# Performance work log

Hardware: AMD Instinct MI355X
Metric: run time of the kernel (lower is better)

Reference implementation:

```python
import jax, jax.numpy as jnp
import numpy as np

ALPHA = 0.2  # dt/tau leaky-integration constant from the module (self._alpha)


def setup_inputs() -> dict:
    key = jax.random.key(0)
    ks = jax.random.split(key, 4)
    B, T, I, H, O = 64, 2048, 128, 512, 64
    inputs = jax.random.normal(ks[0], (B, T, I), dtype=jnp.float32)
    # Xavier-ish scales for weights
    W_in = jax.random.normal(ks[1], (H, I), dtype=jnp.float32) / np.sqrt(I)
    b_in = jnp.zeros((H,), dtype=jnp.float32)
    W_rec = jax.random.normal(ks[2], (H, H), dtype=jnp.float32) * (1.2 / np.sqrt(H))
    h_bias = jnp.zeros((H,), dtype=jnp.float32)
    W_out = jax.random.normal(ks[3], (O, H), dtype=jnp.float32) * (0.1 / np.sqrt(H))
    b_out = jnp.zeros((O,), dtype=jnp.float32)
    return {"inputs": inputs, "W_in": W_in, "b_in": b_in, "W_rec": W_rec,
            "h_bias": h_bias, "W_out": W_out, "b_out": b_out}


def reference(inputs, W_in, b_in, W_rec, h_bias, W_out, b_out):
    # inputs: [B, T, I] -> outputs: [B, T, O]
    B, T, I = inputs.shape
    H = W_rec.shape[0]
    # Precompute input projection for all timesteps: [B, T, H]
    x_proj = jnp.einsum('bti,hi->bth', inputs, W_in) + b_in
    h0 = jnp.zeros((B, H), dtype=inputs.dtype)

    def step(h, xp_t):
        # xp_t: [B, H] precomputed input_proj(x_t)
        h_raw = jnp.tanh(xp_t + h @ W_rec.T + h_bias)
        h_new = (1.0 - ALPHA) * h + ALPHA * h_raw
        return h_new, h_new

    # scan over time-major input projections
    _, hs = jax.lax.scan(step, h0, jnp.swapaxes(x_proj, 0, 1))  # hs: [T, B, H]
    hs = jnp.swapaxes(hs, 0, 1)  # [B, T, H]
    outputs = jnp.einsum('bth,oh->bto', hs, W_out) + b_out
    return outputs
```

## Files before the change

kernel.cpp:

```cpp
#include <hip/hip_runtime.h>


#define TT 2048
#define II 128
#define HH 512
#define OO 64

typedef unsigned long long u64;

union PW { u64 u; float f[2]; unsigned w[2]; };

__device__ __forceinline__ float dot4(float acc, float4 a, float4 w) {
    acc = fmaf(a.x, w.x, acc);
    acc = fmaf(a.y, w.y, acc);
    acc = fmaf(a.z, w.z, acc);
    acc = fmaf(a.w, w.w, acc);
    return acc;
}

__device__ __forceinline__ float fast_tanh(float x) {
    float ax = fabsf(x);
    float e  = __expf(-2.0f * ax);
    float r  = (1.0f - e) * __builtin_amdgcn_rcpf(1.0f + e);
    return copysignf(r, x);
}

__launch_bounds__(512, 1)
__global__ void rnn_persistent(const float* __restrict__ inputs,
                               const float* __restrict__ W_in,
                               const float* __restrict__ b_in,
                               const float* __restrict__ W_rec,
                               const float* __restrict__ h_bias,
                               const float* __restrict__ W_out,
                               const float* __restrict__ b_out,
                               float* __restrict__ out,
                               u64* __restrict__ gbufs)
{
    const int tid = (int)threadIdx.x;
    const int bid = (int)blockIdx.x;

    const int xcd = bid & 7;
    const int idx = bid >> 3;
    const int c   = idx & 3;
    const int g   = xcd * 8 + (idx >> 2);

    u64* gb0 = gbufs + (size_t)g * 1024;

    const int ksl = tid & 7;
    const int jp  = tid >> 3;
    const int j0  = c * 128 + jp * 2;
    const int j1  = j0 + 1;
    const int o   = c * 16 + (tid >> 5);
    const int ol  = tid & 31;

    __shared__ __align__(16) float hx[2][8][68];
    __shared__ __align__(16) float xt[2][8][20];

    float4 wr0[16], wr1[16];
#pragma unroll
    for (int q = 0; q < 16; ++q) {
        wr0[q] = *(const float4*)(W_rec + (size_t)j0 * HH + ksl * 64 + q * 4);
        wr1[q] = *(const float4*)(W_rec + (size_t)j1 * HH + ksl * 64 + q * 4);
    }
    float4 wi0[4], wi1[4];
#pragma unroll
    for (int q = 0; q < 4; ++q) {
        wi0[q] = *(const float4*)(W_in + (size_t)j0 * II + ksl * 16 + q * 4);
        wi1[q] = *(const float4*)(W_in + (size_t)j1 * II + ksl * 16 + q * 4);
    }
    float4 wo[4];
#pragma unroll
    for (int q = 0; q < 4; ++q)
        wo[q] = *(const float4*)(W_out + (size_t)o * HH + ol * 16 + q * 4);

    const float bias0 = b_in[j0] + h_bias[j0];
    const float bias1 = b_in[j1] + h_bias[j1];
    const float bo    = b_out[o];

    hx[0][tid >> 6][tid & 63] = 0.f;

    float hp0 = 0.f, hp1 = 0.f;

    const float* xptr = inputs + (size_t)g * TT * II + (tid & 127);
    float xv = 0.f;
    if (tid < 128) {
        xt[0][tid >> 4][tid & 15] = xptr[0];
        xv = xptr[II];
    }

    const int gm = (((c + 1 + (tid >> 7)) & 3) << 7) | (tid & 127);

    long budget = 1L << 20;

    __syncthreads();

    for (int t = 0; t < TT; ++t) {
        const int p = t & 1;
        u64* gb = gb0 + p * 512;
        const unsigned tag = (unsigned)(t + 1);

        float a0 = 0.f, a1 = 0.f;
        {
            const float4* hc = (const float4*)&hx[p][ksl][0];
#pragma unroll
            for (int q = 0; q < 16; ++q) {
                const float4 hv = hc[q];
                a0 = dot4(a0, hv, wr0[q]);
                a1 = dot4(a1, hv, wr1[q]);
            }
        }
        {
            const float4* xc = (const float4*)&xt[p][ksl][0];
#pragma unroll
            for (int q = 0; q < 4; ++q) {
                const float4 x4 = xc[q];
                a0 = dot4(a0, x4, wi0[q]);
                a1 = dot4(a1, x4, wi1[q]);
            }
        }
#pragma unroll
        for (int m = 1; m < 8; m <<= 1) {
            a0 += __shfl_xor(a0, m);
            a1 += __shfl_xor(a1, m);
        }

        hp0 = 0.8f * hp0 + 0.2f * fast_tanh(a0 + bias0);
        hp1 = 0.8f * hp1 + 0.2f * fast_tanh(a1 + bias1);

        if (ksl == 0) {
            PW w; w.f[0] = hp0; w.w[1] = tag;
            __hip_atomic_store(gb + j0, w.u, __ATOMIC_RELAXED, __HIP_MEMORY_SCOPE_AGENT);
        } else if (ksl == 1) {
            PW w; w.f[0] = hp1; w.w[1] = tag;
            __hip_atomic_store(gb + j1, w.u, __ATOMIC_RELAXED, __HIP_MEMORY_SCOPE_AGENT);
        } else if (ksl == 2) {
            float* dst = &hx[p ^ 1][j0 >> 6][j0 & 63];
            dst[0] = hp0;
            dst[1] = hp1;
        }
        asm volatile("" ::: "memory");

        if (t > 0) {
            float po = 0.f;
            const float4* hq = (const float4*)&hx[p][ol >> 2][(ol & 3) * 16];
#pragma unroll
            for (int q = 0; q < 4; ++q) po = dot4(po, hq[q], wo[q]);
#pragma unroll
            for (int m = 1; m < 32; m <<= 1) po += __shfl_xor(po, m);
            if (ol == 0) out[((size_t)g * TT + (t - 1)) * OO + o] = po + bo;
        }

        if (tid < 128) {
            xt[p ^ 1][tid >> 4][tid & 15] = xv;
            const int tn = (t + 2 < TT) ? (t + 2) : (TT - 1);
            xv = xptr[(size_t)tn * II];
        }

        if (tid < 384) {
            const u64* src = gb + gm;
            PW w;
            w.u = __hip_atomic_load(src, __ATOMIC_RELAXED, __HIP_MEMORY_SCOPE_AGENT);
            while (w.w[1] != tag) {
                __builtin_amdgcn_s_sleep(1);
                w.u = __hip_atomic_load(src, __ATOMIC_RELAXED, __HIP_MEMORY_SCOPE_AGENT);
                if (--budget < 0) break;
            }
            hx[p ^ 1][gm >> 6][gm & 63] = w.f[0];
        }
        __syncthreads();
    }

    {
        float po = 0.f;
        const float4* hq = (const float4*)&hx[0][ol >> 2][(ol & 3) * 16];
#pragma unroll
        for (int q = 0; q < 4; ++q) po = dot4(po, hq[q], wo[q]);
#pragma unroll
        for (int m = 1; m < 32; m <<= 1) po += __shfl_xor(po, m);
        if (ol == 0) out[((size_t)g * TT + (TT - 1)) * OO + o] = po + bo;
    }
}

extern "C" void kernel_launch(void* const* d_in, const int* in_sizes, int n_in,
                              void* d_out, int out_size, void* d_ws, size_t ws_size,
                              hipStream_t stream) {
    const float* inputs = (const float*)d_in[0];
    const float* W_in   = (const float*)d_in[1];
    const float* b_in   = (const float*)d_in[2];
    const float* W_rec  = (const float*)d_in[3];
    const float* h_bias = (const float*)d_in[4];
    const float* W_out  = (const float*)d_in[5];
    const float* b_out  = (const float*)d_in[6];
    float* out = (float*)d_out;

    u64* gbufs = (u64*)d_ws;
    hipMemsetAsync(d_ws, 0, 64 * 2 * 512 * sizeof(u64), stream);
    rnn_persistent<<<256, 512, 0, stream>>>(inputs, W_in, b_in, W_rec, h_bias,
                                            W_out, b_out, out, gbufs);
}
```

Before: 3.464 ms.

## Switch RNN state, weights and exchange to fp16 with fdot2 accumulation

Converts the register-resident weights, the shared hidden-state and input tiles, and the cross-block exchanged hidden values to fp16, and does the dot products with fdot2 (fp32 accumulation). Each global exchange word now packs two hidden values plus the tag, which halves the number of polling threads and spin loads per step. The sleep in the spin-wait is also removed to cut handoff latency. Storing the recurrent state in fp16 over 2048 steps risks accumulated precision error.

```diff
diff --git a/kernel.cpp b/kernel.cpp
--- a/kernel.cpp
+++ b/kernel.cpp
@@ -7,15 +7,28 @@
 #define OO 64
 
 typedef unsigned long long u64;
-
-union PW { u64 u; float f[2]; unsigned w[2]; };
-
-__device__ __forceinline__ float dot4(float acc, float4 a, float4 w) {
-    acc = fmaf(a.x, w.x, acc);
-    acc = fmaf(a.y, w.y, acc);
-    acc = fmaf(a.z, w.z, acc);
-    acc = fmaf(a.w, w.w, acc);
+typedef _Float16 h2_t __attribute__((ext_vector_type(2)));
+typedef _Float16 h8_t __attribute__((ext_vector_type(8)));
+
+union PW { u64 u; unsigned w[2]; _Float16 h[4]; };
+
+__device__ __forceinline__ float dot8(float acc, h8_t a, h8_t b) {
+    h2_t a0 = {a[0], a[1]}, a1 = {a[2], a[3]}, a2 = {a[4], a[5]}, a3 = {a[6], a[7]};
+    h2_t b0 = {b[0], b[1]}, b1 = {b[2], b[3]}, b2 = {b[4], b[5]}, b3 = {b[6], b[7]};
+    acc = __builtin_amdgcn_fdot2(a0, b0, acc, false);
+    acc = __builtin_amdgcn_fdot2(a1, b1, acc, false);
+    acc = __builtin_amdgcn_fdot2(a2, b2, acc, false);
+    acc = __builtin_amdgcn_fdot2(a3, b3, acc, false);
     return acc;
+}
+
+__device__ __forceinline__ h8_t cvt8(const float* p) {
+    const float4 lo = *(const float4*)p;
+    const float4 hi = *(const float4*)(p + 4);
+    h8_t r;
+    r[0] = (_Float16)lo.x; r[1] = (_Float16)lo.y; r[2] = (_Float16)lo.z; r[3] = (_Float16)lo.w;
+    r[4] = (_Float16)hi.x; r[5] = (_Float16)hi.y; r[6] = (_Float16)hi.z; r[7] = (_Float16)hi.w;
+    return r;
 }
 
 __device__ __forceinline__ float fast_tanh(float x) {
@@ -44,7 +57,7 @@
     const int c   = idx & 3;
     const int g   = xcd * 8 + (idx >> 2);
 
-    u64* gb0 = gbufs + (size_t)g * 1024;
+    u64* gb0 = gbufs + (size_t)g * 512;
 
     const int ksl = tid & 7;
     const int jp  = tid >> 3;
@@ -53,42 +66,43 @@
     const int o   = c * 16 + (tid >> 5);
     const int ol  = tid & 31;
 
-    __shared__ __align__(16) float hx[2][8][68];
-    __shared__ __align__(16) float xt[2][8][20];
-
-    float4 wr0[16], wr1[16];
-#pragma unroll
-    for (int q = 0; q < 16; ++q) {
-        wr0[q] = *(const float4*)(W_rec + (size_t)j0 * HH + ksl * 64 + q * 4);
-        wr1[q] = *(const float4*)(W_rec + (size_t)j1 * HH + ksl * 64 + q * 4);
-    }
-    float4 wi0[4], wi1[4];
-#pragma unroll
-    for (int q = 0; q < 4; ++q) {
-        wi0[q] = *(const float4*)(W_in + (size_t)j0 * II + ksl * 16 + q * 4);
-        wi1[q] = *(const float4*)(W_in + (size_t)j1 * II + ksl * 16 + q * 4);
-    }
-    float4 wo[4];
-#pragma unroll
-    for (int q = 0; q < 4; ++q)
-        wo[q] = *(const float4*)(W_out + (size_t)o * HH + ol * 16 + q * 4);
+    __shared__ __align__(16) _Float16 hx[2][8][72];
+    __shared__ __align__(16) _Float16 xt[2][8][24];
+
+    h8_t wr0[8], wr1[8];
+#pragma unroll
+    for (int q = 0; q < 8; ++q) {
+        wr0[q] = cvt8(W_rec + (size_t)j0 * HH + ksl * 64 + q * 8);
+        wr1[q] = cvt8(W_rec + (size_t)j1 * HH + ksl * 64 + q * 8);
+    }
+    h8_t wi0[2], wi1[2];
+#pragma unroll
+    for (int q = 0; q < 2; ++q) {
+        wi0[q] = cvt8(W_in + (size_t)j0 * II + ksl * 16 + q * 8);
+        wi1[q] = cvt8(W_in + (size_t)j1 * II + ksl * 16 + q * 8);
+    }
+    h8_t wo[2];
+#pragma unroll
+    for (int q = 0; q < 2; ++q)
+        wo[q] = cvt8(W_out + (size_t)o * HH + ol * 16 + q * 8);
 
     const float bias0 = b_in[j0] + h_bias[j0];
     const float bias1 = b_in[j1] + h_bias[j1];
     const float bo    = b_out[o];
 
-    hx[0][tid >> 6][tid & 63] = 0.f;
+    if (tid < 288) ((unsigned*)&hx[0][0][0])[tid] = 0u;
 
     float hp0 = 0.f, hp1 = 0.f;
 
-    const float* xptr = inputs + (size_t)g * TT * II + (tid & 127);
+    const int xi = tid & 127;
+    const float* xptr = inputs + (size_t)g * TT * II + xi;
     float xv = 0.f;
     if (tid < 128) {
-        xt[0][tid >> 4][tid & 15] = xptr[0];
+        xt[0][xi >> 4][xi & 15] = (_Float16)xptr[0];
         xv = xptr[II];
     }
 
-    const int gm = (((c + 1 + (tid >> 7)) & 3) << 7) | (tid & 127);
+    const int gm = (((c + 1 + (tid >> 6)) & 3) << 6) | (tid & 63);
 
     long budget = 1L << 20;
 
@@ -96,26 +110,26 @@
 
     for (int t = 0; t < TT; ++t) {
         const int p = t & 1;
-        u64* gb = gb0 + p * 512;
+        u64* gb = gb0 + p * 256;
         const unsigned tag = (unsigned)(t + 1);
 
         float a0 = 0.f, a1 = 0.f;
         {
-            const float4* hc = (const float4*)&hx[p][ksl][0];
-#pragma unroll
-            for (int q = 0; q < 16; ++q) {
-                const float4 hv = hc[q];
-                a0 = dot4(a0, hv, wr0[q]);
-                a1 = dot4(a1, hv, wr1[q]);
+            const h8_t* hc = (const h8_t*)&hx[p][ksl][0];
+#pragma unroll
+            for (int q = 0; q < 8; ++q) {
+                const h8_t hv = hc[q];
+                a0 = dot8(a0, hv, wr0[q]);
+                a1 = dot8(a1, hv, wr1[q]);
             }
         }
         {
-            const float4* xc = (const float4*)&xt[p][ksl][0];
-#pragma unroll
-            for (int q = 0; q < 4; ++q) {
-                const float4 x4 = xc[q];
-                a0 = dot4(a0, x4, wi0[q]);
-                a1 = dot4(a1, x4, wi1[q]);
+            const h8_t* xc = (const h8_t*)&xt[p][ksl][0];
+#pragma unroll
+            for (int q = 0; q < 2; ++q) {
+                const h8_t x8 = xc[q];
+                a0 = dot8(a0, x8, wi0[q]);
+                a1 = dot8(a1, x8, wi1[q]);
             }
         }
 #pragma unroll
@@ -128,53 +142,53 @@
         hp1 = 0.8f * hp1 + 0.2f * fast_tanh(a1 + bias1);
 
         if (ksl == 0) {
-            PW w; w.f[0] = hp0; w.w[1] = tag;
-            __hip_atomic_store(gb + j0, w.u, __ATOMIC_RELAXED, __HIP_MEMORY_SCOPE_AGENT);
-        } else if (ksl == 1) {
-            PW w; w.f[0] = hp1; w.w[1] = tag;
-            __hip_atomic_store(gb + j1, w.u, __ATOMIC_RELAXED, __HIP_MEMORY_SCOPE_AGENT);
+            PW w;
+            w.h[0] = (_Float16)hp0;
+            w.h[1] = (_Float16)hp1;
+            w.w[1] = tag;
+            __hip_atomic_store(gb + ((j0) >> 1), w.u,
+                               __ATOMIC_RELAXED, __HIP_MEMORY_SCOPE_AGENT);
         } else if (ksl == 2) {
-            float* dst = &hx[p ^ 1][j0 >> 6][j0 & 63];
-            dst[0] = hp0;
-            dst[1] = hp1;
+            h2_t v = {(_Float16)hp0, (_Float16)hp1};
+            *(h2_t*)&hx[p ^ 1][j0 >> 6][j0 & 63] = v;
         }
         asm volatile("" ::: "memory");
 
         if (t > 0) {
             float po = 0.f;
-            const float4* hq = (const float4*)&hx[p][ol >> 2][(ol & 3) * 16];
-#pragma unroll
-            for (int q = 0; q < 4; ++q) po = dot4(po, hq[q], wo[q]);
+            const h8_t* hq = (const h8_t*)&hx[p][ol >> 2][(ol & 3) * 16];
+            po = dot8(po, hq[0], wo[0]);
+            po = dot8(po, hq[1], wo[1]);
 #pragma unroll
             for (int m = 1; m < 32; m <<= 1) po += __shfl_xor(po, m);
             if (ol == 0) out[((size_t)g * TT + (t - 1)) * OO + o] = po + bo;
         }
 
         if (tid < 128) {
-            xt[p ^ 1][tid >> 4][tid & 15] = xv;
+            xt[p ^ 1][xi >> 4][xi & 15] = (_Float16)xv;
             const int tn = (t + 2 < TT) ? (t + 2) : (TT - 1);
             xv = xptr[(size_t)tn * II];
         }
 
-        if (tid < 384) {
+        if (tid < 192) {
             const u64* src = gb + gm;
             PW w;
             w.u = __hip_atomic_load(src, __ATOMIC_RELAXED, __HIP_MEMORY_SCOPE_AGENT);
             while (w.w[1] != tag) {
-                __builtin_amdgcn_s_sleep(1);
                 w.u = __hip_atomic_load(src, __ATOMIC_RELAXED, __HIP_MEMORY_SCOPE_AGENT);
                 if (--budget < 0) break;
             }
-            hx[p ^ 1][gm >> 6][gm & 63] = w.f[0];
+            const int j = gm * 2;
+            *(h2_t*)&hx[p ^ 1][j >> 6][j & 63] = *(const h2_t*)&w.h[0];
         }
         __syncthreads();
     }
 
     {
         float po = 0.f;
-        const float4* hq = (const float4*)&hx[0][ol >> 2][(ol & 3) * 16];
-#pragma unroll
-        for (int q = 0; q < 4; ++q) po = dot4(po, hq[q], wo[q]);
+        const h8_t* hq = (const h8_t*)&hx[0][ol >> 2][(ol & 3) * 16];
+        po = dot8(po, hq[0], wo[0]);
+        po = dot8(po, hq[1], wo[1]);
 #pragma unroll
         for (int m = 1; m < 32; m <<= 1) po += __shfl_xor(po, m);
         if (ol == 0) out[((size_t)g * TT + (TT - 1)) * OO + o] = po + bo;
@@ -194,7 +208,7 @@
     float* out = (float*)d_out;
 
     u64* gbufs = (u64*)d_ws;
-    hipMemsetAsync(d_ws, 0, 64 * 2 * 512 * sizeof(u64), stream);
+    hipMemsetAsync(d_ws, 0, 64 * 2 * 256 * sizeof(u64), stream);
     rnn_persistent<<<256, 512, 0, stream>>>(inputs, W_in, b_in, W_rec, h_bias,
                                             W_out, b_out, out, gbufs);
 }
```

New measurement: 2.928 ms. 1.18x faster.
